# Kernel tuning notes

Hardware: AMD Instinct MI355X
Metric: run time of the kernel (lower is better)

## Reference

```python
import jax, jax.numpy as jnp
import numpy as np

DIN = 256
HID = 512

def setup_inputs() -> dict:
    key = jax.random.key(0)
    ks = jax.random.split(key, 9)
    s_in = 1.0 / np.sqrt(DIN)
    s_h = 1.0 / np.sqrt(HID)
    h = jax.random.normal(ks[0], (32, 1024, DIN), dtype=jnp.float32)
    Wv = jax.random.uniform(ks[1], (HID, DIN), jnp.float32, -s_in, s_in)
    bv = jax.random.uniform(ks[2], (HID,), jnp.float32, -s_in, s_in)
    Wk = jax.random.uniform(ks[3], (HID, DIN), jnp.float32, -s_in, s_in)
    bk = jax.random.uniform(ks[4], (HID,), jnp.float32, -s_in, s_in)
    Wq = jax.random.uniform(ks[5], (HID, DIN), jnp.float32, -s_in, s_in)
    bq = jax.random.uniform(ks[6], (HID,), jnp.float32, -s_in, s_in)
    Wo = jax.random.uniform(ks[7], (DIN, HID), jnp.float32, -s_h, s_h)
    bo = jax.random.uniform(ks[8], (DIN,), jnp.float32, -s_h, s_h)
    return {"h": h, "Wv": Wv, "bv": bv, "Wk": Wk, "bk": bk, "Wq": Wq, "bq": bq, "Wo": Wo, "bo": bo}

def reference(h, Wv, bv, Wk, bk, Wq, bq, Wo, bo):
    # relu-activated Q/K/V projections: [B, N, HID]
    v = jax.nn.relu(jnp.einsum('bnd,hd->bnh', h, Wv) + bv)
    q = jax.nn.relu(jnp.einsum('bnd,hd->bnh', h, Wq) + bq)
    k = jax.nn.relu(jnp.einsum('bnd,hd->bnh', h, Wk) + bk)
    # unscaled attention: [B, N, N]
    att = jax.nn.softmax(jnp.einsum('bnh,bmh->bnm', q, k), axis=2)
    out = jnp.einsum('bnm,bmh->bnh', att, v)          # [B, N, HID]
    out = jax.nn.relu(jnp.einsum('bnh,dh->bnd', out, Wo) + bo)  # [B, N, DIN]
    return out
```

## Files before the change

kernel.cpp:

```cpp
#include <hip/hip_runtime.h>
#include <cstdint>
#include <cstddef>

#define NB    32
#define SEQ   1024
#define DIN   256
#define HID   512
#define MTOT  32768

typedef _Float16 half_t;
typedef _Float16 half8  __attribute__((ext_vector_type(8)));
typedef _Float16 half4v __attribute__((ext_vector_type(4)));
typedef float    f32x4  __attribute__((ext_vector_type(4)));

typedef __attribute__((address_space(1))) const void* gas_ptr;
typedef __attribute__((address_space(3))) void*       las_ptr;


__global__ void cvt_kernel(const float* __restrict__ src, half_t* __restrict__ dst, int n4) {
    int i = blockIdx.x * blockDim.x + threadIdx.x;
    if (i < n4) {
        f32x4 v = ((const f32x4*)src)[i];
        half4v h;
        h[0] = (half_t)v[0]; h[1] = (half_t)v[1]; h[2] = (half_t)v[2]; h[3] = (half_t)v[3];
        ((half4v*)dst)[i] = h;
    }
}

__global__ void cvt4_kernel(const float* __restrict__ s0, const float* __restrict__ s1,
                            const float* __restrict__ s2, const float* __restrict__ s3,
                            half_t* __restrict__ d0, half_t* __restrict__ d1,
                            half_t* __restrict__ d2, half_t* __restrict__ d3, int n4) {
    int y = blockIdx.y;
    const float* s = y == 0 ? s0 : y == 1 ? s1 : y == 2 ? s2 : s3;
    half_t*      d = y == 0 ? d0 : y == 1 ? d1 : y == 2 ? d2 : d3;
    int i = blockIdx.x * blockDim.x + threadIdx.x;
    if (i < n4) {
        f32x4 v = ((const f32x4*)s)[i];
        half4v h;
        h[0] = (half_t)v[0]; h[1] = (half_t)v[1]; h[2] = (half_t)v[2]; h[3] = (half_t)v[3];
        ((half4v*)d)[i] = h;
    }
}

__global__ void pack_bias(const float* __restrict__ bv, const float* __restrict__ bk,
                          const float* __restrict__ bq, float* __restrict__ dst) {
    int t = threadIdx.x;
    if (t < HID) {
        dst[t]         = bv[t];
        dst[HID + t]   = bk[t];
        dst[2*HID + t] = bq[t];
    }
}

template<int MODE>
__global__ __launch_bounds__(256, 2) void gemm_k(
    const half_t* __restrict__ A, long lda, long a_bs,
    const half_t* __restrict__ Bw, long ldb, long b_bs,
    void* __restrict__ Out, long ldo, long o_bs,
    const float* __restrict__ bias,
    int Kdim, half_t* __restrict__ out2)
{
    __shared__ alignas(16) half_t As[2][128 * 32];
    __shared__ alignas(16) half_t Bs[2][128 * 32];

    const int t    = threadIdx.x;
    const int lane = t & 63;
    const int wave = t >> 6;
    const int wm   = wave >> 1;
    const int wn   = wave & 1;
    const int lanen = lane & 15;
    const int quad  = lane >> 4;
    const int sl    = quad ^ ((lanen >> 1) & 3);
    const int z     = blockIdx.z;
    const long m0 = (long)blockIdx.x * 128;
    const long n0 = (long)blockIdx.y * 128;

    const half_t* Ab = A  + (long)z * a_bs;
    const half_t* Bb = Bw + (long)z * b_bs;

    f32x4 acc[4][4];
#pragma unroll
    for (int i = 0; i < 4; i++)
#pragma unroll
        for (int j = 0; j < 4; j++)
            acc[i][j] = f32x4{0.f, 0.f, 0.f, 0.f};

    const int c0 = t, c1 = t + 256;
    const int r0 = c0 >> 2, kc0 = (c0 & 3) ^ ((c0 >> 3) & 3);
    const int r1 = c1 >> 2, kc1 = (c1 & 3) ^ ((c1 >> 3) & 3);

    const half_t* gA0 = Ab + (m0 + r0) * lda + kc0 * 8;
    const half_t* gA1 = Ab + (m0 + r1) * lda + kc1 * 8;
    const half_t* gB0 = Bb + (n0 + r0) * ldb + kc0 * 8;
    const half_t* gB1 = Bb + (n0 + r1) * ldb + kc1 * 8;
    const int lA0 = c0 * 8, lA1 = c1 * 8;
    const int lB0 = c0 * 8, lB1 = c1 * 8;

    int aoff[4], boff[4];
#pragma unroll
    for (int i = 0; i < 4; i++) aoff[i] = (wm * 64 + i * 16 + lanen) * 32 + sl * 8;
#pragma unroll
    for (int j = 0; j < 4; j++) boff[j] = (wn * 64 + j * 16 + lanen) * 32 + sl * 8;

    for (int k0 = 0; k0 < Kdim; k0 += 64) {
#pragma unroll
        for (int sub = 0; sub < 2; sub++) {
            const int ks = k0 + sub * 32;
            __builtin_amdgcn_global_load_lds((gas_ptr)(gA0 + ks), (las_ptr)&As[sub][lA0], 16, 0, 0);
            __builtin_amdgcn_global_load_lds((gas_ptr)(gA1 + ks), (las_ptr)&As[sub][lA1], 16, 0, 0);
            __builtin_amdgcn_global_load_lds((gas_ptr)(gB0 + ks), (las_ptr)&Bs[sub][lB0], 16, 0, 0);
            __builtin_amdgcn_global_load_lds((gas_ptr)(gB1 + ks), (las_ptr)&Bs[sub][lB1], 16, 0, 0);
        }
        __syncthreads();

        {
            half8 af[4], bf[4];
#pragma unroll
            for (int i = 0; i < 4; i++) af[i] = *(const half8*)&As[0][aoff[i]];
#pragma unroll
            for (int j = 0; j < 4; j++) bf[j] = *(const half8*)&Bs[0][boff[j]];
#pragma unroll
            for (int i = 0; i < 4; i++)
#pragma unroll
                for (int j = 0; j < 4; j++)
                    acc[i][j] = __builtin_amdgcn_mfma_f32_16x16x32_f16(af[i], bf[j], acc[i][j], 0, 0, 0);
        }
        {
            half8 af[4], bf[4];
#pragma unroll
            for (int i = 0; i < 4; i++) af[i] = *(const half8*)&As[1][aoff[i]];
#pragma unroll
            for (int j = 0; j < 4; j++) bf[j] = *(const half8*)&Bs[1][boff[j]];
#pragma unroll
            for (int i = 0; i < 4; i++)
#pragma unroll
                for (int j = 0; j < 4; j++)
                    acc[i][j] = __builtin_amdgcn_mfma_f32_16x16x32_f16(af[i], bf[j], acc[i][j], 0, 0, 0);
        }
        __syncthreads();
    }

#pragma unroll
    for (int i = 0; i < 4; i++) {
        long mrow = m0 + wm * 64 + i * 16 + quad * 4;
#pragma unroll
        for (int j = 0; j < 4; j++) {
            long gn = n0 + wn * 64 + j * 16 + lanen;
            f32x4 v = acc[i][j];
            if (MODE == 0) {
                float bb = bias[z * HID + gn];
                half_t h0 = (half_t)fmaxf(v[0] + bb, 0.f);
                half_t h1 = (half_t)fmaxf(v[1] + bb, 0.f);
                half_t h2 = (half_t)fmaxf(v[2] + bb, 0.f);
                half_t h3 = (half_t)fmaxf(v[3] + bb, 0.f);
                if (z == 0) {
                    long bidx = mrow >> 10;
                    long pos  = mrow & 1023;
                    half4v pk; pk[0] = h0; pk[1] = h1; pk[2] = h2; pk[3] = h3;
                    *(half4v*)(out2 + ((bidx * HID + gn) << 10) + pos) = pk;
                } else {
                    half_t* o = (half_t*)Out + (long)(z - 1) * o_bs;
                    o[(mrow + 0) * ldo + gn] = h0;
                    o[(mrow + 1) * ldo + gn] = h1;
                    o[(mrow + 2) * ldo + gn] = h2;
                    o[(mrow + 3) * ldo + gn] = h3;
                }
            } else {
                float* o = (float*)Out;
                float bb = bias[gn];
#pragma unroll
                for (int r = 0; r < 4; r++) o[(mrow + r) * ldo + gn] = fmaxf(v[r] + bb, 0.f);
            }
        }
    }
}

template<int SWZ>
__global__ __launch_bounds__(256, 3) void se_k(
    const half_t* __restrict__ Q, const half_t* __restrict__ K,
    half_t* __restrict__ E, float* __restrict__ Mstat, float* __restrict__ Lstat)
{
    __shared__ alignas(16) half_t As[2][128 * 32];
    __shared__ alignas(16) half_t Bs[2][128 * 32];

    const int t    = threadIdx.x;
    const int lane = t & 63;
    const int wm   = t >> 6;
    const int lanen = lane & 15;
    const int quad  = lane >> 4;

    int bx, by, z;
    if (SWZ) {
        const int wgid = blockIdx.x;
        const int c    = wgid & 7;
        const int tmp  = wgid >> 3;
        const int tile = tmp & 63;
        z  = c + 8 * (tmp >> 6);
        bx = tile & 7;
        by = tile >> 3;
    } else {
        bx = blockIdx.x; by = blockIdx.y; z = blockIdx.z;
    }
    const long m0 = (long)bx * 128;
    const long n0 = (long)by * 128;

    const half_t* Ab = Q + (long)z * SEQ * HID;
    const half_t* Bb = K + (long)z * SEQ * HID;

    f32x4 acc[2][8];
#pragma unroll
    for (int i = 0; i < 2; i++)
#pragma unroll
        for (int j = 0; j < 8; j++)
            acc[i][j] = f32x4{0.f, 0.f, 0.f, 0.f};

    const half_t* gA[2]; int lA[2];
    const half_t* gB[2]; int lB[2];
#pragma unroll
    for (int s = 0; s < 2; s++) {
        int c = t + 256 * s;
        gA[s] = Ab + (m0 + (c >> 2)) * HID + (c & 3) * 8;
        gB[s] = Bb + (n0 + (c >> 2)) * HID + (c & 3) * 8;
        lA[s] = c * 8;
        lB[s] = c * 8;
    }

    int aoff[2], boff[8];
#pragma unroll
    for (int i = 0; i < 2; i++) aoff[i] = (wm * 32 + i * 16 + lanen) * 32 + quad * 8;
#pragma unroll
    for (int j = 0; j < 8; j++) boff[j] = (j * 16 + lanen) * 32 + quad * 8;

    for (int k0 = 0; k0 < HID; k0 += 64) {
#pragma unroll
        for (int sub = 0; sub < 2; sub++) {
            const int ks = k0 + sub * 32;
#pragma unroll
            for (int s = 0; s < 2; s++) {
                __builtin_amdgcn_global_load_lds((gas_ptr)(gA[s] + ks), (las_ptr)&As[sub][lA[s]], 16, 0, 0);
                __builtin_amdgcn_global_load_lds((gas_ptr)(gB[s] + ks), (las_ptr)&Bs[sub][lB[s]], 16, 0, 0);
            }
        }
        __syncthreads();

#pragma unroll
        for (int sub = 0; sub < 2; sub++) {
            half8 af0 = *(const half8*)&As[sub][aoff[0]];
            half8 af1 = *(const half8*)&As[sub][aoff[1]];
#pragma unroll
            for (int j = 0; j < 8; j++) {
                half8 bf = *(const half8*)&Bs[sub][boff[j]];
                acc[0][j] = __builtin_amdgcn_mfma_f32_16x16x32_f16(af0, bf, acc[0][j], 0, 0, 0);
                acc[1][j] = __builtin_amdgcn_mfma_f32_16x16x32_f16(af1, bf, acc[1][j], 0, 0, 0);
            }
        }
        __syncthreads();
    }

    float mf[2][4];
#pragma unroll
    for (int i = 0; i < 2; i++)
#pragma unroll
        for (int r = 0; r < 4; r++) {
            float v = acc[i][0][r];
#pragma unroll
            for (int j = 1; j < 8; j++) v = fmaxf(v, acc[i][j][r]);
#pragma unroll
            for (int off = 8; off > 0; off >>= 1)
                v = fmaxf(v, __shfl_xor(v, off, 64));
            mf[i][r] = v;
        }

    half_t* Eb = E + (long)z * SEQ * SEQ;
    float rs[2][4];
#pragma unroll
    for (int i = 0; i < 2; i++)
#pragma unroll
        for (int r = 0; r < 4; r++) rs[i][r] = 0.f;
#pragma unroll
    for (int i = 0; i < 2; i++) {
        long mrow = m0 + wm * 32 + i * 16 + quad * 4;
#pragma unroll
        for (int j = 0; j < 8; j++) {
            long gn = n0 + j * 16 + lanen;
#pragma unroll
            for (int r = 0; r < 4; r++) {
                float e = __expf(acc[i][j][r] - mf[i][r]);
                rs[i][r] += e;
                Eb[(mrow + r) * SEQ + gn] = (half_t)e;
            }
        }
    }
#pragma unroll
    for (int i = 0; i < 2; i++)
#pragma unroll
        for (int r = 0; r < 4; r++) {
            float v = rs[i][r];
#pragma unroll
            for (int off = 8; off > 0; off >>= 1)
                v += __shfl_xor(v, off, 64);
            rs[i][r] = v;
        }

    if (lanen == 0) {
        long base = ((long)z * 8 + by) * SEQ + m0 + wm * 32;
#pragma unroll
        for (int i = 0; i < 2; i++)
#pragma unroll
            for (int r = 0; r < 4; r++) {
                Mstat[base + i * 16 + quad * 4 + r] = mf[i][r];
                Lstat[base + i * 16 + quad * 4 + r] = rs[i][r];
            }
    }
}

template<int SWZ>
__global__ __launch_bounds__(256, 2) void pv_k(
    const half_t* __restrict__ E, const half_t* __restrict__ vT,
    const float* __restrict__ Mstat, const float* __restrict__ Lstat,
    half_t* __restrict__ O16)
{
    __shared__ alignas(16) half_t As[2][128 * 32];
    __shared__ alignas(16) half_t Bs[2][256 * 32];
    __shared__ float scaleS[8][128];
    __shared__ float invS[128];

    const int t    = threadIdx.x;
    const int lane = t & 63;
    const int wave = t >> 6;
    const int wm   = wave >> 1;
    const int wn   = wave & 1;
    const int lanen = lane & 15;
    const int quad  = lane >> 4;
    const int sl    = quad ^ ((lanen >> 1) & 3);

    int bx, by, z;
    if (SWZ) {
        const int wgid = blockIdx.x;
        const int c    = wgid & 7;
        const int tmp  = wgid >> 3;
        const int tile = tmp & 15;
        z  = c + 8 * (tmp >> 4);
        bx = tile & 7;
        by = tile >> 3;
    } else {
        bx = blockIdx.x; by = blockIdx.y; z = blockIdx.z;
    }
    const long m0 = (long)bx * 128;
    const long h0 = (long)by * 256;

    if (t < 128) {
        float mv[8];
        float M = -1e30f;
#pragma unroll
        for (int kb = 0; kb < 8; kb++) {
            mv[kb] = Mstat[((long)z * 8 + kb) * SEQ + m0 + t];
            M = fmaxf(M, mv[kb]);
        }
        float ls = 0.f;
#pragma unroll
        for (int kb = 0; kb < 8; kb++) {
            float sc = __expf(mv[kb] - M);
            scaleS[kb][t] = sc;
            ls += Lstat[((long)z * 8 + kb) * SEQ + m0 + t] * sc;
        }
        invS[t] = 1.f / ls;
    }
    __syncthreads();

    const half_t* Ab = E  + (long)z * SEQ * SEQ;
    const half_t* Bb = vT + (long)z * HID * SEQ;

    f32x4 acc[4][8];
#pragma unroll
    for (int i = 0; i < 4; i++)
#pragma unroll
        for (int j = 0; j < 8; j++)
            acc[i][j] = f32x4{0.f, 0.f, 0.f, 0.f};

    const half_t* gA[2]; int lA[2];
    const half_t* gB[4]; int lB[4];
#pragma unroll
    for (int s = 0; s < 2; s++) {
        int c = t + 256 * s;
        gA[s] = Ab + (m0 + (c >> 2)) * SEQ + ((c & 3) ^ ((c >> 3) & 3)) * 8;
        lA[s] = c * 8;
    }
#pragma unroll
    for (int s = 0; s < 4; s++) {
        int c = t + 256 * s;
        gB[s] = Bb + (h0 + (c >> 2)) * SEQ + ((c & 3) ^ ((c >> 3) & 3)) * 8;
        lB[s] = c * 8;
    }

    int aoff[4], boff[8];
#pragma unroll
    for (int i = 0; i < 4; i++) aoff[i] = (wm * 64 + i * 16 + lanen) * 32 + sl * 8;
#pragma unroll
    for (int j = 0; j < 8; j++) boff[j] = (wn * 128 + j * 16 + lanen) * 32 + sl * 8;

    for (int k0 = 0; k0 < SEQ; k0 += 64) {
#pragma unroll
        for (int sub = 0; sub < 2; sub++) {
            const int ks = k0 + sub * 32;
#pragma unroll
            for (int s = 0; s < 2; s++)
                __builtin_amdgcn_global_load_lds((gas_ptr)(gA[s] + ks), (las_ptr)&As[sub][lA[s]], 16, 0, 0);
#pragma unroll
            for (int s = 0; s < 4; s++)
                __builtin_amdgcn_global_load_lds((gas_ptr)(gB[s] + ks), (las_ptr)&Bs[sub][lB[s]], 16, 0, 0);
        }
        __syncthreads();

        const int kb = k0 >> 7;
        {
            half8 af[4], bf[8];
#pragma unroll
            for (int i = 0; i < 4; i++) {
                af[i] = *(const half8*)&As[0][aoff[i]];
                half_t sh = (half_t)scaleS[kb][wm * 64 + i * 16 + lanen];
                af[i] *= sh;
            }
#pragma unroll
            for (int j = 0; j < 8; j++) bf[j] = *(const half8*)&Bs[0][boff[j]];
#pragma unroll
            for (int i = 0; i < 4; i++)
#pragma unroll
                for (int j = 0; j < 8; j++)
                    acc[i][j] = __builtin_amdgcn_mfma_f32_16x16x32_f16(af[i], bf[j], acc[i][j], 0, 0, 0);
        }
        {
            half8 af[4], bf[8];
#pragma unroll
            for (int i = 0; i < 4; i++) {
                af[i] = *(const half8*)&As[1][aoff[i]];
                half_t sh = (half_t)scaleS[kb][wm * 64 + i * 16 + lanen];
                af[i] *= sh;
            }
#pragma unroll
            for (int j = 0; j < 8; j++) bf[j] = *(const half8*)&Bs[1][boff[j]];
#pragma unroll
            for (int i = 0; i < 4; i++)
#pragma unroll
                for (int j = 0; j < 8; j++)
                    acc[i][j] = __builtin_amdgcn_mfma_f32_16x16x32_f16(af[i], bf[j], acc[i][j], 0, 0, 0);
        }
        __syncthreads();
    }

    half_t* o = O16 + (long)z * SEQ * HID;
#pragma unroll
    for (int i = 0; i < 4; i++) {
        long mrow = m0 + wm * 64 + i * 16 + quad * 4;
        int rl = wm * 64 + i * 16 + quad * 4;
#pragma unroll
        for (int j = 0; j < 8; j++) {
            long gn = h0 + wn * 128 + j * 16 + lanen;
#pragma unroll
            for (int r = 0; r < 4; r++)
                o[(mrow + r) * HID + gn] = (half_t)(acc[i][j][r] * invS[rl + r]);
        }
    }
}

extern "C" void kernel_launch(void* const* d_in, const int* in_sizes, int n_in,
                              void* d_out, int out_size, void* d_ws, size_t ws_size,
                              hipStream_t stream) {
    const float* h  = (const float*)d_in[0];
    const float* Wv = (const float*)d_in[1];
    const float* bv = (const float*)d_in[2];
    const float* Wk = (const float*)d_in[3];
    const float* bk = (const float*)d_in[4];
    const float* Wq = (const float*)d_in[5];
    const float* bq = (const float*)d_in[6];
    const float* Wo = (const float*)d_in[7];
    const float* bo = (const float*)d_in[8];

    uint8_t* ws = (uint8_t*)d_ws;
    size_t off = 0;
    auto alloc = [&](size_t bytes) { size_t o = off; off += (bytes + 255) & ~(size_t)255; return o; };

    half_t* W16   = (half_t*)(ws + alloc((size_t)3 * HID * DIN * 2));
    half_t* Wo16  = (half_t*)(ws + alloc((size_t)DIN * HID * 2));
    float*  biasq = (float*)(ws + alloc((size_t)3 * HID * 4));
    half_t* k16   = (half_t*)(ws + alloc((size_t)MTOT * HID * 2));
    half_t* q16   = (half_t*)(ws + alloc((size_t)MTOT * HID * 2));
    half_t* vT    = (half_t*)(ws + alloc((size_t)MTOT * HID * 2));
    size_t h16_off = alloc((size_t)MTOT * DIN * 2);
    half_t* h16   = (half_t*)(ws + h16_off);
    half_t* O16 = q16;

    size_t s_avail = ws_size > h16_off ? ws_size - h16_off : 0;
    size_t per_batch = (size_t)SEQ * SEQ * 2 + 2 * 8 * SEQ * 4;
    int GB = (int)(s_avail / per_batch);
    if (GB < 1)  GB = 1;
    if (GB > NB) GB = NB;
    half_t* Ebuf  = (half_t*)(ws + h16_off);
    float*  Mstat = (float*)(ws + h16_off + (size_t)GB * SEQ * SEQ * 2);
    float*  Lstat = Mstat + (size_t)GB * 8 * SEQ;

    cvt_kernel<<<dim3((MTOT * DIN / 4 + 255) / 256), 256, 0, stream>>>(h, h16, MTOT * DIN / 4);
    cvt4_kernel<<<dim3((HID * DIN / 4 + 255) / 256, 4), 256, 0, stream>>>(
        Wv, Wk, Wq, Wo, W16, W16 + HID * DIN, W16 + 2 * HID * DIN, Wo16, HID * DIN / 4);
    pack_bias<<<dim3(1), 512, 0, stream>>>(bv, bk, bq, biasq);

    gemm_k<0><<<dim3(MTOT / 128, HID / 128, 3), 256, 0, stream>>>(
        h16, DIN, 0,
        W16, DIN, (long)HID * DIN,
        (void*)k16, HID, (long)MTOT * HID,
        biasq, DIN, vT);

    if (GB == NB) {
        se_k<1><<<dim3(NB * 64), 256, 0, stream>>>(q16, k16, Ebuf, Mstat, Lstat);
        pv_k<1><<<dim3(NB * 16), 256, 0, stream>>>(Ebuf, vT, Mstat, Lstat, O16);
    } else {
        for (int g0 = 0; g0 < NB; g0 += GB) {
            int gb = NB - g0 < GB ? NB - g0 : GB;
            se_k<0><<<dim3(SEQ / 128, SEQ / 128, gb), 256, 0, stream>>>(
                q16 + (size_t)g0 * SEQ * HID,
                k16 + (size_t)g0 * SEQ * HID,
                Ebuf, Mstat, Lstat);
            pv_k<0><<<dim3(SEQ / 128, HID / 256, gb), 256, 0, stream>>>(
                Ebuf, vT + (size_t)g0 * HID * SEQ,
                Mstat, Lstat,
                O16 + (size_t)g0 * SEQ * HID);
        }
    }

    gemm_k<3><<<dim3(MTOT / 128, DIN / 128, 1), 256, 0, stream>>>(
        O16, HID, 0,
        Wo16, HID, 0,
        d_out, DIN, 0,
        bo, HID, nullptr);

    (void)in_sizes; (void)n_in; (void)out_size;
}
```

Measured before the change: 265.7 us.

## Shrink PV tile to 128x128, double grid, raise occupancy bounds

The P·V kernel tile shrinks from 128x256 to 128x128 output columns. Each of the four waves now owns 32 rows across all 128 columns, and the launch grid doubles to 1024 workgroups. Launch bounds for gemm_k and pv_k rise from 2 to 3 blocks per CU, aiming at more parallelism and occupancy with fewer accumulator registers. The cost is that each tile of the E matrix is now read twice as often from global memory, and tighter register limits on gemm_k may cause spills.

```diff
diff --git a/kernel.cpp b/kernel.cpp
--- a/kernel.cpp
+++ b/kernel.cpp
@@ -54,7 +54,7 @@
 }
 
 template<int MODE>
-__global__ __launch_bounds__(256, 2) void gemm_k(
+__global__ __launch_bounds__(256, 3) void gemm_k(
     const half_t* __restrict__ A, long lda, long a_bs,
     const half_t* __restrict__ Bw, long ldb, long b_bs,
     void* __restrict__ Out, long ldo, long o_bs,
@@ -316,21 +316,19 @@
 }
 
 template<int SWZ>
-__global__ __launch_bounds__(256, 2) void pv_k(
+__global__ __launch_bounds__(256, 3) void pv_k(
     const half_t* __restrict__ E, const half_t* __restrict__ vT,
     const float* __restrict__ Mstat, const float* __restrict__ Lstat,
     half_t* __restrict__ O16)
 {
     __shared__ alignas(16) half_t As[2][128 * 32];
-    __shared__ alignas(16) half_t Bs[2][256 * 32];
+    __shared__ alignas(16) half_t Bs[2][128 * 32];
     __shared__ float scaleS[8][128];
     __shared__ float invS[128];
 
     const int t    = threadIdx.x;
     const int lane = t & 63;
-    const int wave = t >> 6;
-    const int wm   = wave >> 1;
-    const int wn   = wave & 1;
+    const int wm   = t >> 6;
     const int lanen = lane & 15;
     const int quad  = lane >> 4;
     const int sl    = quad ^ ((lanen >> 1) & 3);
@@ -340,15 +338,15 @@
         const int wgid = blockIdx.x;
         const int c    = wgid & 7;
         const int tmp  = wgid >> 3;
-        const int tile = tmp & 15;
-        z  = c + 8 * (tmp >> 4);
+        const int tile = tmp & 31;
+        z  = c + 8 * (tmp >> 5);
         bx = tile & 7;
         by = tile >> 3;
     } else {
         bx = blockIdx.x; by = blockIdx.y; z = blockIdx.z;
     }
     const long m0 = (long)bx * 128;
-    const long h0 = (long)by * 256;
+    const long h0 = (long)by * 128;
 
     if (t < 128) {
         float mv[8];
@@ -372,91 +370,67 @@
     const half_t* Ab = E  + (long)z * SEQ * SEQ;
     const half_t* Bb = vT + (long)z * HID * SEQ;
 
-    f32x4 acc[4][8];
-#pragma unroll
-    for (int i = 0; i < 4; i++)
+    f32x4 acc[2][8];
+#pragma unroll
+    for (int i = 0; i < 2; i++)
 #pragma unroll
         for (int j = 0; j < 8; j++)
             acc[i][j] = f32x4{0.f, 0.f, 0.f, 0.f};
 
     const half_t* gA[2]; int lA[2];
-    const half_t* gB[4]; int lB[4];
+    const half_t* gB[2]; int lB[2];
 #pragma unroll
     for (int s = 0; s < 2; s++) {
         int c = t + 256 * s;
         gA[s] = Ab + (m0 + (c >> 2)) * SEQ + ((c & 3) ^ ((c >> 3) & 3)) * 8;
+        gB[s] = Bb + (h0 + (c >> 2)) * SEQ + ((c & 3) ^ ((c >> 3) & 3)) * 8;
         lA[s] = c * 8;
-    }
-#pragma unroll
-    for (int s = 0; s < 4; s++) {
-        int c = t + 256 * s;
-        gB[s] = Bb + (h0 + (c >> 2)) * SEQ + ((c & 3) ^ ((c >> 3) & 3)) * 8;
         lB[s] = c * 8;
     }
 
-    int aoff[4], boff[8];
-#pragma unroll
-    for (int i = 0; i < 4; i++) aoff[i] = (wm * 64 + i * 16 + lanen) * 32 + sl * 8;
-#pragma unroll
-    for (int j = 0; j < 8; j++) boff[j] = (wn * 128 + j * 16 + lanen) * 32 + sl * 8;
+    int aoff[2], boff[8];
+#pragma unroll
+    for (int i = 0; i < 2; i++) aoff[i] = (wm * 32 + i * 16 + lanen) * 32 + sl * 8;
+#pragma unroll
+    for (int j = 0; j < 8; j++) boff[j] = (j * 16 + lanen) * 32 + sl * 8;
 
     for (int k0 = 0; k0 < SEQ; k0 += 64) {
 #pragma unroll
         for (int sub = 0; sub < 2; sub++) {
             const int ks = k0 + sub * 32;
 #pragma unroll
-            for (int s = 0; s < 2; s++)
+            for (int s = 0; s < 2; s++) {
                 __builtin_amdgcn_global_load_lds((gas_ptr)(gA[s] + ks), (las_ptr)&As[sub][lA[s]], 16, 0, 0);
-#pragma unroll
-            for (int s = 0; s < 4; s++)
                 __builtin_amdgcn_global_load_lds((gas_ptr)(gB[s] + ks), (las_ptr)&Bs[sub][lB[s]], 16, 0, 0);
+            }
         }
         __syncthreads();
 
         const int kb = k0 >> 7;
-        {
-            half8 af[4], bf[8];
-#pragma unroll
-            for (int i = 0; i < 4; i++) {
-                af[i] = *(const half8*)&As[0][aoff[i]];
-                half_t sh = (half_t)scaleS[kb][wm * 64 + i * 16 + lanen];
-                af[i] *= sh;
-            }
-#pragma unroll
-            for (int j = 0; j < 8; j++) bf[j] = *(const half8*)&Bs[0][boff[j]];
-#pragma unroll
-            for (int i = 0; i < 4; i++)
-#pragma unroll
-                for (int j = 0; j < 8; j++)
-                    acc[i][j] = __builtin_amdgcn_mfma_f32_16x16x32_f16(af[i], bf[j], acc[i][j], 0, 0, 0);
-        }
-        {
-            half8 af[4], bf[8];
-#pragma unroll
-            for (int i = 0; i < 4; i++) {
-                af[i] = *(const half8*)&As[1][aoff[i]];
-                half_t sh = (half_t)scaleS[kb][wm * 64 + i * 16 + lanen];
-                af[i] *= sh;
-            }
-#pragma unroll
-            for (int j = 0; j < 8; j++) bf[j] = *(const half8*)&Bs[1][boff[j]];
-#pragma unroll
-            for (int i = 0; i < 4; i++)
-#pragma unroll
-                for (int j = 0; j < 8; j++)
-                    acc[i][j] = __builtin_amdgcn_mfma_f32_16x16x32_f16(af[i], bf[j], acc[i][j], 0, 0, 0);
+#pragma unroll
+        for (int sub = 0; sub < 2; sub++) {
+            half8 af0 = *(const half8*)&As[sub][aoff[0]];
+            half8 af1 = *(const half8*)&As[sub][aoff[1]];
+            af0 *= (half_t)scaleS[kb][wm * 32 + 0 * 16 + lanen];
+            af1 *= (half_t)scaleS[kb][wm * 32 + 1 * 16 + lanen];
+#pragma unroll
+            for (int j = 0; j < 8; j++) {
+                half8 bf = *(const half8*)&Bs[sub][boff[j]];
+                acc[0][j] = __builtin_amdgcn_mfma_f32_16x16x32_f16(af0, bf, acc[0][j], 0, 0, 0);
+                acc[1][j] = __builtin_amdgcn_mfma_f32_16x16x32_f16(af1, bf, acc[1][j], 0, 0, 0);
+            }
         }
         __syncthreads();
     }
 
     half_t* o = O16 + (long)z * SEQ * HID;
 #pragma unroll
-    for (int i = 0; i < 4; i++) {
-        long mrow = m0 + wm * 64 + i * 16 + quad * 4;
-        int rl = wm * 64 + i * 16 + quad * 4;
+    for (int i = 0; i < 2; i++) {
+        long mrow = m0 + wm * 32 + i * 16 + quad * 4;
+        int rl = wm * 32 + i * 16 + quad * 4;
 #pragma unroll
         for (int j = 0; j < 8; j++) {
-            long gn = h0 + wn * 128 + j * 16 + lanen;
+            long gn = h0 + j * 16 + lanen;
 #pragma unroll
             for (int r = 0; r < 4; r++)
                 o[(mrow + r) * HID + gn] = (half_t)(acc[i][j][r] * invS[rl + r]);
@@ -513,7 +487,7 @@
 
     if (GB == NB) {
         se_k<1><<<dim3(NB * 64), 256, 0, stream>>>(q16, k16, Ebuf, Mstat, Lstat);
-        pv_k<1><<<dim3(NB * 16), 256, 0, stream>>>(Ebuf, vT, Mstat, Lstat, O16);
+        pv_k<1><<<dim3(NB * 32), 256, 0, stream>>>(Ebuf, vT, Mstat, Lstat, O16);
     } else {
         for (int g0 = 0; g0 < NB; g0 += GB) {
             int gb = NB - g0 < GB ? NB - g0 : GB;
@@ -521,7 +495,7 @@
                 q16 + (size_t)g0 * SEQ * HID,
                 k16 + (size_t)g0 * SEQ * HID,
                 Ebuf, Mstat, Lstat);
-            pv_k<0><<<dim3(SEQ / 128, HID / 256, gb), 256, 0, stream>>>(
+            pv_k<0><<<dim3(SEQ / 128, HID / 128, gb), 256, 0, stream>>>(
                 Ebuf, vT + (size_t)g0 * HID * SEQ,
                 Mstat, Lstat,
                 O16 + (size_t)g0 * SEQ * HID);
```

New measurement: 269.0 us. No clear change (+1.3%).
